# Kernel optimization log

Measured on AMD Instinct MI355X. Metric: run time of the kernel, lower is better.

The kernel has to match this reference:

```python
import jax, jax.numpy as jnp
import numpy as np

B, S, D, H = 2, 2048, 1024, 16
MAX_DIST = 1024


def setup_inputs() -> dict:
    key = jax.random.key(0)
    ks = jax.random.split(key, 7)
    w = lambda k, shape: jax.random.normal(k, shape, jnp.float32) * 0.02
    return {
        "x": jax.random.normal(ks[0], (B, S, D), jnp.float32),
        "Wq": w(ks[1], (D, D)), "bq": jnp.zeros((D,), jnp.float32),
        "Wk": w(ks[2], (D, D)),
        "Wv": w(ks[3], (D, D)), "bv": jnp.zeros((D,), jnp.float32),
        "Wo": w(ks[4], (D, D)), "bo": jnp.zeros((D,), jnp.float32),
        "pos_bias": w(ks[5], (2 * MAX_DIST - 1, H)),
        "max_dist": MAX_DIST,
    }


def reference(x, Wq, bq, Wk, Wv, bv, Wo, bo, pos_bias, max_dist):
    b, s, d_model = x.shape
    h = pos_bias.shape[1]
    hd = d_model // h  # head dim
    scale = hd ** -0.25  # module's scale applied to (QK^T + rel_bias)

    split = lambda t: t.reshape(b, s, h, hd).transpose(0, 2, 1, 3)  # [b,h,s,hd]
    q = split(x @ Wq + bq)
    k = split(x @ Wk)          # key has no bias
    v = split(x @ Wv + bv)

    # raw QK^T (unscaled), as in the module
    scores = jnp.einsum('bhqd,bhkd->bhqk', q, k)

    # relative-position bias gather: clamp(i-j) -> table index
    pos = jnp.arange(s)[:, None] - jnp.arange(s)[None, :]
    pos = jnp.clip(pos, -max_dist + 1, max_dist - 1) + max_dist - 1
    rel_bias = pos_bias[pos].transpose(2, 0, 1)[None]  # [1,h,s,s]

    # SDPA with attn_mask = (scores + rel_bias)*scale adds it on top of QK^T/sqrt(hd)
    logits = scores * (1.0 / jnp.sqrt(jnp.float32(hd))) + (scores + rel_bias) * scale
    w = jax.nn.softmax(logits, axis=-1)

    out = jnp.einsum('bhqk,bhkd->bhqd', w, v)
    out = out.transpose(0, 2, 1, 3).reshape(b, s, d_model)
    return out @ Wo + bo
```

## Files before the change

### kernel.cpp

```cpp
#include <hip/hip_runtime.h>
#include <hip/hip_bf16.h>
#include <cstddef>
#include <cstdint>

#define BATCH   2
#define S_LEN   2048
#define D_MODEL 1024
#define NH      16
#define HD      64
#define MAXD    1024

#define SCORE_SCALE 0.47855339059327373f
#define BIAS_SCALE  0.35355339059327373f
#define FIXM 8.0f
#define LOG2E 1.4426950408889634f

typedef __attribute__((ext_vector_type(8))) short bf16x8;
typedef __attribute__((ext_vector_type(4))) short bf16x4;
typedef __attribute__((ext_vector_type(4))) float f32x4;

static __device__ __forceinline__ unsigned short f2bf(float f) {
    __hip_bfloat16 h = __float2bfloat16(f);
    return *reinterpret_cast<unsigned short*>(&h);
}

#define GLDS(gp, lp) __builtin_amdgcn_global_load_lds( \
    (const __attribute__((address_space(1))) void*)(gp), \
    (__attribute__((address_space(3))) void*)(lp), 16, 0, 0)

__global__ __launch_bounds__(256) void prep(
    const float* __restrict__ x,
    const float* __restrict__ Wq, const float* __restrict__ Wk,
    const float* __restrict__ Wv, const float* __restrict__ Wo,
    const float* __restrict__ pos_bias,
    unsigned short* __restrict__ xb, unsigned short* __restrict__ Wqkvt,
    unsigned short* __restrict__ Wot,
    float* __restrict__ pb_t)
{
    __shared__ float t[32][33];
    const int bx = blockIdx.x, tid = threadIdx.x;

    if (bx < 2048) {
        const size_t i = ((size_t)bx * 256 + tid) * 8;
        const float4 a = *(const float4*)(x + i);
        const float4 b = *(const float4*)(x + i + 4);
        unsigned short u[8] = {f2bf(a.x), f2bf(a.y), f2bf(a.z), f2bf(a.w),
                               f2bf(b.x), f2bf(b.y), f2bf(b.z), f2bf(b.w)};
        *(uint4*)(xb + i) = *(const uint4*)u;
    } else if (bx < 6144) {
        const int bx2 = bx - 2048;
        const int z = bx2 >> 10, inner = bx2 & 1023;
        const int gx = inner & 31, gy = inner >> 5;
        const float* W = (z == 0) ? Wq : (z == 1) ? Wk : (z == 2) ? Wv : Wo;
        unsigned short* hi = (z < 3) ? Wqkvt + (size_t)z * 1024 * 1024 : Wot;
        const int bxx = gx * 32, byy = gy * 32;
        const int tx = tid & 31, ty = tid >> 5;
        #pragma unroll
        for (int i = 0; i < 4; i++)
            t[ty + 8 * i][tx] = W[(size_t)(byy + ty + 8 * i) * 1024 + bxx + tx];
        __syncthreads();
        #pragma unroll
        for (int i = 0; i < 4; i++) {
            const float v = t[tx][ty + 8 * i];
            const size_t o = (size_t)(bxx + ty + 8 * i) * 1024 + byy + tx;
            hi[o] = f2bf(v);
        }
    } else {
        const int o0 = (bx - 6144) * 1024 + tid * 4;
        float v[4];
        #pragma unroll
        for (int j = 0; j < 4; j++) {
            const int o = o0 + j;
            const int hh = o >> 12, ii = o & 4095;
            int rel = ii - 2047;
            rel = min(max(rel, -(MAXD - 1)), MAXD - 1);
            v[j] = (BIAS_SCALE * pos_bias[(size_t)(rel + MAXD - 1) * NH + hh] - FIXM) * LOG2E;
        }
        *(float4*)&pb_t[o0] = *(const float4*)v;
    }
}

#define GBM 128
#define GBN 128
#define GBK 32

__global__ __launch_bounds__(256) void gemm_qkv(
    const unsigned short* __restrict__ A, const unsigned short* __restrict__ Bt,
    const float* __restrict__ bq, const float* __restrict__ bv,
    unsigned short* __restrict__ Cout)
{
    const int K = 1024;
    __shared__ __align__(16) unsigned short As[GBM][GBK];
    __shared__ __align__(16) unsigned short Bs[GBN][GBK];

    const int tid = threadIdx.x;
    const int wave = tid >> 6, lane = tid & 63;
    const int quad = lane >> 4, cl = lane & 15;
    const int wm = (wave & 1) * 64, wn = (wave >> 1) * 64;
    const int bm = blockIdx.y * GBM, bn = blockIdx.x * GBN;

    const int sr = wave * 32 + (lane >> 2);
    const int sc = (lane & 3) * 8;
    const unsigned short* aS0 = A  + (size_t)(bm + sr) * K + sc;
    const unsigned short* aS1 = aS0 + (size_t)16 * K;
    const unsigned short* bS0 = Bt + (size_t)(bn + sr) * K + sc;
    const unsigned short* bS1 = bS0 + (size_t)16 * K;
    unsigned short* aD0 = &As[wave * 32][0];
    unsigned short* aD1 = &As[wave * 32 + 16][0];
    unsigned short* bD0 = &Bs[wave * 32][0];
    unsigned short* bD1 = &Bs[wave * 32 + 16][0];

    f32x4 acc[4][4];
    #pragma unroll
    for (int mi = 0; mi < 4; mi++)
        #pragma unroll
        for (int ni = 0; ni < 4; ni++)
            #pragma unroll
            for (int r = 0; r < 4; r++) acc[mi][ni][r] = 0.f;

    for (int k0 = 0; k0 < K; k0 += GBK) {
        __syncthreads();
        GLDS(aS0, aD0); GLDS(aS1, aD1);
        GLDS(bS0, bD0); GLDS(bS1, bD1);
        aS0 += GBK; aS1 += GBK; bS0 += GBK; bS1 += GBK;
        __syncthreads();

        bf16x8 af[4], bf[4];
        #pragma unroll
        for (int mi = 0; mi < 4; mi++)
            af[mi] = *(const bf16x8*)&As[wm + mi * 16 + cl][quad * 8];
        #pragma unroll
        for (int ni = 0; ni < 4; ni++)
            bf[ni] = *(const bf16x8*)&Bs[wn + ni * 16 + cl][quad * 8];
        #pragma unroll
        for (int mi = 0; mi < 4; mi++)
            #pragma unroll
            for (int ni = 0; ni < 4; ni++)
                acc[mi][ni] = __builtin_amdgcn_mfma_f32_16x16x32_bf16(
                    af[mi], bf[ni], acc[mi][ni], 0, 0, 0);
    }

    #pragma unroll
    for (int ni = 0; ni < 4; ni++) {
        const int coln = bn + wn + ni * 16 + cl;
        const int region = coln >> 10, c = coln & 1023;
        const float bs = (region == 0) ? bq[c] : (region == 2) ? bv[c] : 0.f;
        #pragma unroll
        for (int mi = 0; mi < 4; mi++) {
            const int row0 = bm + wm + mi * 16 + quad * 4;
            if (region == 2) {
                const int hh = c >> 6, d = c & 63;
                const int bb = row0 >> 11, s0 = row0 & 2047;
                unsigned short u[4];
                #pragma unroll
                for (int r = 0; r < 4; r++) u[r] = f2bf(acc[mi][ni][r] + bs);
                unsigned short* dst = Cout + (size_t)8 * 1024 * 1024
                    + (((size_t)bb * NH + hh) * HD + d) * S_LEN + s0;
                *(uint2*)dst = *(const uint2*)u;
            } else {
                unsigned short* dst = Cout + (size_t)region * 4 * 1024 * 1024;
                #pragma unroll
                for (int r = 0; r < 4; r++)
                    dst[(size_t)(row0 + r) * 1024 + c] = f2bf(acc[mi][ni][r] + bs);
            }
        }
    }
}

#define TQB 128
#define TKB 64

__global__ __launch_bounds__(512, 4) void attn_mfma(
    const unsigned short* __restrict__ Q, const unsigned short* __restrict__ K,
    const unsigned short* __restrict__ VT, const float* __restrict__ pb_t,
    unsigned short* __restrict__ O)
{
    const int qt = blockIdx.x, h = blockIdx.y, b = blockIdx.z;
    const int tid  = threadIdx.x;
    const int wave = tid >> 6, lane = tid & 63;
    const int g = wave >> 2, w4 = wave & 3;
    const int quad = lane >> 4, col = lane & 15;
    const int qbase = qt * TQB;
    const int qw = qbase + w4 * 32;

    __shared__ __align__(16) unsigned char smem[65536];
    unsigned char* const base_g = smem + g * 32768;

    bf16x8 qf[2][2];
    #pragma unroll
    for (int f = 0; f < 2; f++) {
        const unsigned short* qp =
            &Q[((size_t)(b * S_LEN) + qw + f * 16 + col) * D_MODEL + h * HD + quad * 8];
        qf[f][0] = *(const bf16x8*)qp;
        qf[f][1] = *(const bf16x8*)(qp + 32);
    }

    f32x4 accO[2][4];
    #pragma unroll
    for (int f = 0; f < 2; f++)
        #pragma unroll
        for (int nb = 0; nb < 4; nb++)
            #pragma unroll
            for (int r = 0; r < 4; r++) accO[f][nb][r] = 0.f;
    f32x4 accL[2];
    #pragma unroll
    for (int f = 0; f < 2; f++)
        #pragma unroll
        for (int r = 0; r < 4; r++) accL[f][r] = 0.f;
    const bf16x4 vone = {(short)16256, (short)16256, (short)16256, (short)16256};

    const int tg = tid & 255;
    const int s0 = tg, s1 = 256 + tg;
    const int kr0 = s0 >> 3, kj0 = (s0 & 7) ^ (kr0 & 7);
    const int kr1 = s1 >> 3, kj1 = (s1 & 7) ^ (kr1 & 7);
    const unsigned short* kS0 =
        K + ((size_t)(b * S_LEN) + g * 1024 + kr0) * D_MODEL + h * HD + kj0 * 8;
    const unsigned short* kS1 =
        K + ((size_t)(b * S_LEN) + g * 1024 + kr1) * D_MODEL + h * HD + kj1 * 8;
    const size_t vbase = ((size_t)(b * NH + h) * HD) * S_LEN;
    const unsigned short* vS0 = VT + vbase + (size_t)kr0 * S_LEN + g * 1024 + kj0 * 8;
    const unsigned short* vS1 = VT + vbase + (size_t)kr1 * S_LEN + g * 1024 + kj1 * 8;
    unsigned short* kD = (unsigned short*)base_g + w4 * 512;
    unsigned short* vD = (unsigned short*)(base_g + 8192) + w4 * 512;

    const float* pbh = pb_t + h * 4096;
    const float* pb_lane = pbh + (qw + col - quad * 4 - g * 1024 + 2047);
    const float SC2 = SCORE_SCALE * LOG2E;
    const int jsw = col & 7;

    GLDS(kS0, kD); GLDS(kS1, kD + 2048);
    GLDS(vS0, vD); GLDS(vS1, vD + 2048);
    kS0 += (size_t)TKB * D_MODEL; kS1 += (size_t)TKB * D_MODEL;
    vS0 += TKB; vS1 += TKB;
    __syncthreads();

    const int NT = 1024 / TKB;

#define ATT_TILE(T, P)                                                        \
  {                                                                           \
    if ((T) != NT - 1) {                                                      \
      GLDS(kS0, kD + ((P) ^ 1) * 8192); GLDS(kS1, kD + ((P) ^ 1) * 8192 + 2048); \
      GLDS(vS0, vD + ((P) ^ 1) * 8192); GLDS(vS1, vD + ((P) ^ 1) * 8192 + 2048); \
      kS0 += (size_t)TKB * D_MODEL; kS1 += (size_t)TKB * D_MODEL;             \
      vS0 += TKB; vS1 += TKB;                                                 \
    }                                                                         \
    float bias_c[2][16];                                                      \
    _Pragma("unroll")                                                         \
    for (int f = 0; f < 2; f++)                                               \
      _Pragma("unroll")                                                       \
      for (int nb = 0; nb < 4; nb++)                                          \
        _Pragma("unroll")                                                     \
        for (int r = 0; r < 4; r++)                                           \
          bias_c[f][nb * 4 + r] = pb_lane[f * 16 - (nb * 16 + r)];            \
    pb_lane -= TKB;                                                           \
    const unsigned short* Kp = (const unsigned short*)(base_g + (P) * 16384); \
    const unsigned short* Vp = (const unsigned short*)(base_g + (P) * 16384 + 8192); \
    f32x4 accS[2][4];                                                         \
    _Pragma("unroll")                                                         \
    for (int f = 0; f < 2; f++)                                               \
      _Pragma("unroll")                                                       \
      for (int nb = 0; nb < 4; nb++)                                          \
        _Pragma("unroll")                                                     \
        for (int r = 0; r < 4; r++) accS[f][nb][r] = 0.f;                     \
    _Pragma("unroll")                                                         \
    for (int kk = 0; kk < 2; kk++)                                            \
      _Pragma("unroll")                                                       \
      for (int nb = 0; nb < 4; nb++) {                                        \
        const bf16x8 kf = *(const bf16x8*)                                    \
            &Kp[(nb * 16 + col) * 64 + (((kk * 4 + quad) ^ jsw) * 8)];        \
        accS[0][nb] = __builtin_amdgcn_mfma_f32_16x16x32_bf16(                \
            kf, qf[0][kk], accS[0][nb], 0, 0, 0);                             \
        accS[1][nb] = __builtin_amdgcn_mfma_f32_16x16x32_bf16(                \
            kf, qf[1][kk], accS[1][nb], 0, 0, 0);                             \
      }                                                                       \
    bf16x4 pf[2][4];                                                          \
    _Pragma("unroll")                                                         \
    for (int f = 0; f < 2; f++)                                               \
      _Pragma("unroll")                                                       \
      for (int nb = 0; nb < 4; nb++) {                                        \
        float pr[4];                                                          \
        _Pragma("unroll")                                                     \
        for (int r = 0; r < 4; r++)                                           \
          pr[r] = __builtin_amdgcn_exp2f(                                     \
              fmaf(accS[f][nb][r], SC2, bias_c[f][nb * 4 + r]));              \
        const __hip_bfloat162 h0 = __float22bfloat162_rn(make_float2(pr[0], pr[1])); \
        const __hip_bfloat162 h1 = __float22bfloat162_rn(make_float2(pr[2], pr[3])); \
        uint2 w;                                                              \
        w.x = *(const unsigned int*)&h0;                                      \
        w.y = *(const unsigned int*)&h1;                                      \
        union { uint2 u; bf16x4 v; } cv;                                      \
        cv.u = w;                                                             \
        pf[f][nb] = cv.v;                                                     \
        accL[f] = __builtin_amdgcn_mfma_f32_16x16x16bf16_1k(                  \
            vone, pf[f][nb], accL[f], 0, 0, 0);                               \
      }                                                                       \
    _Pragma("unroll")                                                         \
    for (int s = 0; s < 4; s++)                                               \
      _Pragma("unroll")                                                       \
      for (int nb = 0; nb < 4; nb++) {                                        \
        const bf16x4 vf = *(const bf16x4*)                                    \
            &Vp[(nb * 16 + col) * 64 + (((2 * s + (quad >> 1)) ^ jsw) * 8) + (quad & 1) * 4]; \
        accO[0][nb] = __builtin_amdgcn_mfma_f32_16x16x16bf16_1k(              \
            vf, pf[0][s], accO[0][nb], 0, 0, 0);                              \
        accO[1][nb] = __builtin_amdgcn_mfma_f32_16x16x16bf16_1k(              \
            vf, pf[1][s], accO[1][nb], 0, 0, 0);                              \
      }                                                                       \
    __syncthreads();                                                          \
  }

    for (int t = 0; t < NT; t += 2) {
        ATT_TILE(t,     0);
        ATT_TILE(t + 1, 1);
    }
#undef ATT_TILE

    float* const Mo = (float*)smem;
    const int idx = (w4 * 64 + lane) * 34;
    if (g == 1) {
        #pragma unroll
        for (int f = 0; f < 2; f++) {
            #pragma unroll
            for (int nb = 0; nb < 4; nb++)
                #pragma unroll
                for (int r = 0; r < 4; r++)
                    Mo[idx + f * 16 + nb * 4 + r] = accO[f][nb][r];
            Mo[idx + 32 + f] = accL[f][0];
        }
    }
    __syncthreads();
    if (g == 0) {
        #pragma unroll
        for (int f = 0; f < 2; f++) {
            const float inv = 1.0f / (accL[f][0] + Mo[idx + 32 + f]);
            const size_t row = (size_t)(b * S_LEN) + qw + f * 16 + col;
            #pragma unroll
            for (int nb = 0; nb < 4; nb++) {
                unsigned short u[4];
                #pragma unroll
                for (int r = 0; r < 4; r++)
                    u[r] = f2bf((accO[f][nb][r] + Mo[idx + f * 16 + nb * 4 + r]) * inv);
                *(uint2*)&O[row * D_MODEL + h * HD + nb * 16 + quad * 4] = *(const uint2*)u;
            }
        }
    }
}

#define OBM 64
#define OBN 128

__global__ __launch_bounds__(256) void gemm_out(
    const unsigned short* __restrict__ A, const unsigned short* __restrict__ Bt,
    const float* __restrict__ bias, float* __restrict__ Cout)
{
    const int N = 1024, Kd = 1024;
    __shared__ __align__(16) unsigned short As[OBM][GBK];
    __shared__ __align__(16) unsigned short Bs[OBN][GBK];

    const int tid = threadIdx.x;
    const int wave = tid >> 6, lane = tid & 63;
    const int quad = lane >> 4, cl = lane & 15;
    const int wm = (wave & 1) * 32, wn = (wave >> 1) * 64;
    const int bm = blockIdx.y * OBM, bn = blockIdx.x * OBN;

    const int ar = tid >> 2, ac = (tid & 3) * 8;
    const unsigned short* aS = A + (size_t)(bm + ar) * Kd + ac;
    const unsigned short* hS0 = Bt + (size_t)(bn + ar) * Kd + ac;
    const unsigned short* hS1 = hS0 + (size_t)64 * Kd;
    unsigned short* aD  = &As[0][0] + wave * 512;
    unsigned short* hD0 = &Bs[0][0] + wave * 512;
    unsigned short* hD1 = hD0 + 2048;

    f32x4 acc[2][4];
    #pragma unroll
    for (int mi = 0; mi < 2; mi++)
        #pragma unroll
        for (int ni = 0; ni < 4; ni++)
            #pragma unroll
            for (int r = 0; r < 4; r++) acc[mi][ni][r] = 0.f;

    for (int k0 = 0; k0 < Kd; k0 += GBK) {
        __syncthreads();
        GLDS(aS, aD);
        GLDS(hS0, hD0); GLDS(hS1, hD1);
        aS += GBK; hS0 += GBK; hS1 += GBK;
        __syncthreads();

        bf16x8 af[2], bh[4];
        #pragma unroll
        for (int mi = 0; mi < 2; mi++)
            af[mi] = *(const bf16x8*)&As[wm + mi * 16 + cl][quad * 8];
        #pragma unroll
        for (int ni = 0; ni < 4; ni++)
            bh[ni] = *(const bf16x8*)&Bs[wn + ni * 16 + cl][quad * 8];
        #pragma unroll
        for (int mi = 0; mi < 2; mi++)
            #pragma unroll
            for (int ni = 0; ni < 4; ni++)
                acc[mi][ni] = __builtin_amdgcn_mfma_f32_16x16x32_bf16(
                    af[mi], bh[ni], acc[mi][ni], 0, 0, 0);
    }

    #pragma unroll
    for (int ni = 0; ni < 4; ni++) {
        const int coln = bn + wn + ni * 16 + cl;
        const float bs = bias[coln];
        #pragma unroll
        for (int mi = 0; mi < 2; mi++) {
            const int row0 = bm + wm + mi * 16 + quad * 4;
            #pragma unroll
            for (int r = 0; r < 4; r++)
                Cout[(size_t)(row0 + r) * N + coln] = acc[mi][ni][r] + bs;
        }
    }
}

extern "C" void kernel_launch(void* const* d_in, const int* in_sizes, int n_in,
                              void* d_out, int out_size, void* d_ws, size_t ws_size,
                              hipStream_t stream)
{
    const float* x        = (const float*)d_in[0];
    const float* Wq       = (const float*)d_in[1];
    const float* bq       = (const float*)d_in[2];
    const float* Wk       = (const float*)d_in[3];
    const float* Wv       = (const float*)d_in[4];
    const float* bv       = (const float*)d_in[5];
    const float* Wo       = (const float*)d_in[6];
    const float* bo       = (const float*)d_in[7];
    const float* pos_bias = (const float*)d_in[8];
    float* out = (float*)d_out;

    const size_t ELEMS  = (size_t)BATCH * S_LEN * D_MODEL;
    const size_t WELEMS = (size_t)D_MODEL * D_MODEL;
    unsigned short* xb     = (unsigned short*)d_ws;
    unsigned short* Wqkvt  = xb + ELEMS;
    unsigned short* Wot    = Wqkvt + 3 * WELEMS;
    unsigned short* QKV    = Wot + WELEMS;
    unsigned short* Qb     = QKV;
    unsigned short* Kb     = Qb + ELEMS;
    unsigned short* VTb    = Kb + ELEMS;
    unsigned short* Ab     = VTb + ELEMS;
    float* pb_t            = (float*)(Ab + ELEMS);

    prep<<<6208, 256, 0, stream>>>(x, Wq, Wk, Wv, Wo, pos_bias,
                                   xb, Wqkvt, Wot, pb_t);

    gemm_qkv<<<dim3(3072 / GBN, 4096 / GBM), 256, 0, stream>>>(
        xb, Wqkvt, bq, bv, QKV);

    attn_mfma<<<dim3(S_LEN / TQB, NH, BATCH), 512, 0, stream>>>(
        Qb, Kb, VTb, pb_t, Ab);

    gemm_out<<<dim3(1024 / OBN, 4096 / OBM), 256, 0, stream>>>(
        Ab, Wot, bo, out);
}
```

Before: 200.4 us.

## Deepen GEMM K tiles with XOR-swizzled LDS, XCD-aware block remap, MFMA priority hints

Both projection GEMMs now stage 64-wide K tiles instead of 32, halving the number of barrier pairs per K loop. The LDS layout is XOR-swizzled on 16-byte chunks to avoid bank conflicts with the wider rows. Block indices are remapped so that consecutive tiles land on the same XCD, which should improve L2 reuse. The attention loop also wraps its MFMA sections in s_setprio hints to favour matrix issue across waves. The cost is twice the LDS per block, which may lower occupancy.

```diff
diff --git a/kernel.cpp b/kernel.cpp
--- a/kernel.cpp
+++ b/kernel.cpp
@@ -82,7 +82,7 @@
 
 #define GBM 128
 #define GBN 128
-#define GBK 32
+#define GBK 64
 
 __global__ __launch_bounds__(256) void gemm_qkv(
     const unsigned short* __restrict__ A, const unsigned short* __restrict__ Bt,
@@ -97,18 +97,22 @@
     const int wave = tid >> 6, lane = tid & 63;
     const int quad = lane >> 4, cl = lane & 15;
     const int wm = (wave & 1) * 64, wn = (wave >> 1) * 64;
-    const int bm = blockIdx.y * GBM, bn = blockIdx.x * GBN;
-
-    const int sr = wave * 32 + (lane >> 2);
-    const int sc = (lane & 3) * 8;
-    const unsigned short* aS0 = A  + (size_t)(bm + sr) * K + sc;
-    const unsigned short* aS1 = aS0 + (size_t)16 * K;
-    const unsigned short* bS0 = Bt + (size_t)(bn + sr) * K + sc;
-    const unsigned short* bS1 = bS0 + (size_t)16 * K;
-    unsigned short* aD0 = &As[wave * 32][0];
-    unsigned short* aD1 = &As[wave * 32 + 16][0];
-    unsigned short* bD0 = &Bs[wave * 32][0];
-    unsigned short* bD1 = &Bs[wave * 32 + 16][0];
+
+    const int gx = gridDim.x;
+    const int nwg = gx * gridDim.y;
+    const int cpx = nwg >> 3;
+    int lin = blockIdx.y * gx + blockIdx.x;
+    lin = (lin & 7) * cpx + (lin >> 3);
+    const int bn = (lin % gx) * GBN;
+    const int bm = (lin / gx) * GBM;
+
+    const int r0 = tid >> 3;
+    const int c0 = ((tid & 7) ^ (r0 & 7)) * 8;
+    const unsigned short* aS = A  + (size_t)(bm + r0) * K + c0;
+    const unsigned short* bS = Bt + (size_t)(bn + r0) * K + c0;
+    unsigned short* aD = &As[0][0] + wave * 512;
+    unsigned short* bD = &Bs[0][0] + wave * 512;
+    const int ksw = cl & 7;
 
     f32x4 acc[4][4];
     #pragma unroll
@@ -120,24 +124,33 @@
 
     for (int k0 = 0; k0 < K; k0 += GBK) {
         __syncthreads();
-        GLDS(aS0, aD0); GLDS(aS1, aD1);
-        GLDS(bS0, bD0); GLDS(bS1, bD1);
-        aS0 += GBK; aS1 += GBK; bS0 += GBK; bS1 += GBK;
+        GLDS(aS,                  aD);
+        GLDS(aS + (size_t)32 * K, aD + 2048);
+        GLDS(aS + (size_t)64 * K, aD + 4096);
+        GLDS(aS + (size_t)96 * K, aD + 6144);
+        GLDS(bS,                  bD);
+        GLDS(bS + (size_t)32 * K, bD + 2048);
+        GLDS(bS + (size_t)64 * K, bD + 4096);
+        GLDS(bS + (size_t)96 * K, bD + 6144);
+        aS += GBK; bS += GBK;
         __syncthreads();
 
-        bf16x8 af[4], bf[4];
-        #pragma unroll
-        for (int mi = 0; mi < 4; mi++)
-            af[mi] = *(const bf16x8*)&As[wm + mi * 16 + cl][quad * 8];
-        #pragma unroll
-        for (int ni = 0; ni < 4; ni++)
-            bf[ni] = *(const bf16x8*)&Bs[wn + ni * 16 + cl][quad * 8];
-        #pragma unroll
-        for (int mi = 0; mi < 4; mi++)
+        #pragma unroll
+        for (int kk = 0; kk < 2; kk++) {
+            bf16x8 af[4], bf[4];
+            #pragma unroll
+            for (int mi = 0; mi < 4; mi++)
+                af[mi] = *(const bf16x8*)&As[wm + mi * 16 + cl][((kk * 4 + quad) ^ ksw) * 8];
             #pragma unroll
             for (int ni = 0; ni < 4; ni++)
-                acc[mi][ni] = __builtin_amdgcn_mfma_f32_16x16x32_bf16(
-                    af[mi], bf[ni], acc[mi][ni], 0, 0, 0);
+                bf[ni] = *(const bf16x8*)&Bs[wn + ni * 16 + cl][((kk * 4 + quad) ^ ksw) * 8];
+            #pragma unroll
+            for (int mi = 0; mi < 4; mi++)
+                #pragma unroll
+                for (int ni = 0; ni < 4; ni++)
+                    acc[mi][ni] = __builtin_amdgcn_mfma_f32_16x16x32_bf16(
+                        af[mi], bf[ni], acc[mi][ni], 0, 0, 0);
+        }
     }
 
     #pragma unroll
@@ -262,6 +275,7 @@
       for (int nb = 0; nb < 4; nb++)                                          \
         _Pragma("unroll")                                                     \
         for (int r = 0; r < 4; r++) accS[f][nb][r] = 0.f;                     \
+    __builtin_amdgcn_s_setprio(1);                                            \
     _Pragma("unroll")                                                         \
     for (int kk = 0; kk < 2; kk++)                                            \
       _Pragma("unroll")                                                       \
@@ -273,6 +287,7 @@
         accS[1][nb] = __builtin_amdgcn_mfma_f32_16x16x32_bf16(                \
             kf, qf[1][kk], accS[1][nb], 0, 0, 0);                             \
       }                                                                       \
+    __builtin_amdgcn_s_setprio(0);                                            \
     bf16x4 pf[2][4];                                                          \
     _Pragma("unroll")                                                         \
     for (int f = 0; f < 2; f++)                                               \
@@ -294,6 +309,7 @@
         accL[f] = __builtin_amdgcn_mfma_f32_16x16x16bf16_1k(                  \
             vone, pf[f][nb], accL[f], 0, 0, 0);                               \
       }                                                                       \
+    __builtin_amdgcn_s_setprio(1);                                            \
     _Pragma("unroll")                                                         \
     for (int s = 0; s < 4; s++)                                               \
       _Pragma("unroll")                                                       \
@@ -305,6 +321,7 @@
         accO[1][nb] = __builtin_amdgcn_mfma_f32_16x16x16bf16_1k(              \
             vf, pf[1][s], accO[1][nb], 0, 0, 0);                              \
       }                                                                       \
+    __builtin_amdgcn_s_setprio(0);                                            \
     __syncthreads();                                                          \
   }
 
@@ -347,28 +364,36 @@
 
 #define OBM 64
 #define OBN 128
+#define OBK 64
 
 __global__ __launch_bounds__(256) void gemm_out(
     const unsigned short* __restrict__ A, const unsigned short* __restrict__ Bt,
     const float* __restrict__ bias, float* __restrict__ Cout)
 {
     const int N = 1024, Kd = 1024;
-    __shared__ __align__(16) unsigned short As[OBM][GBK];
-    __shared__ __align__(16) unsigned short Bs[OBN][GBK];
+    __shared__ __align__(16) unsigned short As[OBM][OBK];
+    __shared__ __align__(16) unsigned short Bs[OBN][OBK];
 
     const int tid = threadIdx.x;
     const int wave = tid >> 6, lane = tid & 63;
     const int quad = lane >> 4, cl = lane & 15;
     const int wm = (wave & 1) * 32, wn = (wave >> 1) * 64;
-    const int bm = blockIdx.y * OBM, bn = blockIdx.x * OBN;
-
-    const int ar = tid >> 2, ac = (tid & 3) * 8;
-    const unsigned short* aS = A + (size_t)(bm + ar) * Kd + ac;
-    const unsigned short* hS0 = Bt + (size_t)(bn + ar) * Kd + ac;
-    const unsigned short* hS1 = hS0 + (size_t)64 * Kd;
-    unsigned short* aD  = &As[0][0] + wave * 512;
-    unsigned short* hD0 = &Bs[0][0] + wave * 512;
-    unsigned short* hD1 = hD0 + 2048;
+
+    const int gx = gridDim.x;
+    const int nwg = gx * gridDim.y;
+    const int cpx = nwg >> 3;
+    int lin = blockIdx.y * gx + blockIdx.x;
+    lin = (lin & 7) * cpx + (lin >> 3);
+    const int bn = (lin % gx) * OBN;
+    const int bm = (lin / gx) * OBM;
+
+    const int r0 = tid >> 3;
+    const int c0 = ((tid & 7) ^ (r0 & 7)) * 8;
+    const unsigned short* aS = A  + (size_t)(bm + r0) * Kd + c0;
+    const unsigned short* bS = Bt + (size_t)(bn + r0) * Kd + c0;
+    unsigned short* aD = &As[0][0] + wave * 512;
+    unsigned short* bD = &Bs[0][0] + wave * 512;
+    const int ksw = cl & 7;
 
     f32x4 acc[2][4];
     #pragma unroll
@@ -378,26 +403,33 @@
             #pragma unroll
             for (int r = 0; r < 4; r++) acc[mi][ni][r] = 0.f;
 
-    for (int k0 = 0; k0 < Kd; k0 += GBK) {
+    for (int k0 = 0; k0 < Kd; k0 += OBK) {
         __syncthreads();
-        GLDS(aS, aD);
-        GLDS(hS0, hD0); GLDS(hS1, hD1);
-        aS += GBK; hS0 += GBK; hS1 += GBK;
+        GLDS(aS,                   aD);
+        GLDS(aS + (size_t)32 * Kd, aD + 2048);
+        GLDS(bS,                   bD);
+        GLDS(bS + (size_t)32 * Kd, bD + 2048);
+        GLDS(bS + (size_t)64 * Kd, bD + 4096);
+        GLDS(bS + (size_t)96 * Kd, bD + 6144);
+        aS += OBK; bS += OBK;
         __syncthreads();
 
-        bf16x8 af[2], bh[4];
-        #pragma unroll
-        for (int mi = 0; mi < 2; mi++)
-            af[mi] = *(const bf16x8*)&As[wm + mi * 16 + cl][quad * 8];
-        #pragma unroll
-        for (int ni = 0; ni < 4; ni++)
-            bh[ni] = *(const bf16x8*)&Bs[wn + ni * 16 + cl][quad * 8];
-        #pragma unroll
-        for (int mi = 0; mi < 2; mi++)
+        #pragma unroll
+        for (int kk = 0; kk < 2; kk++) {
+            bf16x8 af[2], bh[4];
+            #pragma unroll
+            for (int mi = 0; mi < 2; mi++)
+                af[mi] = *(const bf16x8*)&As[wm + mi * 16 + cl][((kk * 4 + quad) ^ ksw) * 8];
             #pragma unroll
             for (int ni = 0; ni < 4; ni++)
-                acc[mi][ni] = __builtin_amdgcn_mfma_f32_16x16x32_bf16(
-                    af[mi], bh[ni], acc[mi][ni], 0, 0, 0);
+                bh[ni] = *(const bf16x8*)&Bs[wn + ni * 16 + cl][((kk * 4 + quad) ^ ksw) * 8];
+            #pragma unroll
+            for (int mi = 0; mi < 2; mi++)
+                #pragma unroll
+                for (int ni = 0; ni < 4; ni++)
+                    acc[mi][ni] = __builtin_amdgcn_mfma_f32_16x16x32_bf16(
+                        af[mi], bh[ni], acc[mi][ni], 0, 0, 0);
+        }
     }
 
     #pragma unroll
```

Measured after the change: 242.0 us. 20.7% more time.
